# Kernel tuning notes

Hardware: AMD Instinct MI355X
Metric: run time of the kernel (lower is better)

Reference implementation:

```python
import jax, jax.numpy as jnp
import numpy as np

LORA_ALPHA = 32.0
LORA_RANK = 16
SCALE = LORA_ALPHA / LORA_RANK  # 2.0


def setup_inputs() -> dict:
    key = jax.random.key(0)
    ks = jax.random.split(key, 6)
    B, S, I, Q, V, E, R = 4, 4096, 4096, 4096, 1024, 8, LORA_RANK
    return {
        "hidden_states": jax.random.normal(ks[0], (B, S, I), dtype=jnp.float32),
        "router_weight": jax.random.normal(ks[1], (E, I), dtype=jnp.float32) * 0.02,
        "q_lora_a": jax.random.normal(ks[2], (E, I, R), dtype=jnp.float32) * 0.02,
        "q_lora_b": jax.random.normal(ks[3], (E, R, Q), dtype=jnp.float32) * 0.02,
        "v_lora_a": jax.random.normal(ks[4], (E, I, R), dtype=jnp.float32) * 0.02,
        "v_lora_b": jax.random.normal(ks[5], (E, R, V), dtype=jnp.float32) * 0.02,
    }


def reference(hidden_states, router_weight, q_lora_a, q_lora_b, v_lora_a, v_lora_b):
    B, S, I = hidden_states.shape
    E = router_weight.shape[0]
    Q = q_lora_b.shape[-1]
    V = v_lora_b.shape[-1]
    h = hidden_states.reshape(-1, I)  # [T, I]

    # Top-1 routing
    logits = h @ router_weight.T                       # [T, E]
    probs = jax.nn.softmax(logits, axis=-1)
    expert_idx = jnp.argmax(probs, axis=-1)            # [T]
    expert_scores = jnp.max(probs, axis=-1)            # [T]

    # One-hot dispatch folded with per-token score * lora scale
    gate = jax.nn.one_hot(expert_idx, E, dtype=h.dtype) * (expert_scores * SCALE)[:, None]  # [T, E]

    # Low-rank projections for all experts (R is tiny so [T,E,R] is cheap),
    # masked so each token only keeps its selected expert.
    low_q = jnp.einsum('ti,eir->ter', h, q_lora_a) * gate[:, :, None]  # [T, E, R]
    low_v = jnp.einsum('ti,eir->ter', h, v_lora_a) * gate[:, :, None]  # [T, E, R]

    q_delta = jnp.einsum('ter,erq->tq', low_q, q_lora_b)  # [T, Q]
    v_delta = jnp.einsum('ter,erv->tv', low_v, v_lora_b)  # [T, V]

    return q_delta.reshape(B, S, Q), v_delta.reshape(B, S, V)
```

## Files before the change

### kernel.cpp

```cpp
#include <hip/hip_runtime.h>
#include <math.h>

#define TOK_I 4096
#define NE 8
#define NR 16
#define NQ 4096
#define NV 1024
#define LORA_SCALE 2.0f

#define BM2 32
#define KB2 128
#define BM3 32

__global__ __launch_bounds__(256) void qvlora_fused_kernel(
    const float* __restrict__ h, const float* __restrict__ rw,
    const float* __restrict__ qa, const float* __restrict__ qb,
    const float* __restrict__ va, const float* __restrict__ vb,
    float* __restrict__ qout, float* __restrict__ vout)
{
    const int tok  = blockIdx.x;
    const int tid  = threadIdx.x;
    const int lane = tid & 63;
    const int wave = tid >> 6;

    __shared__ float red8[4][8];
    __shared__ float red32[4][32];
    __shared__ float sLow[32];
    __shared__ float sGate;
    __shared__ int   sSel;

    const float4* h4 = (const float4*)(h + (long)tok * TOK_I);
    float4 hreg[4];
#pragma unroll
    for (int k = 0; k < 4; ++k) hreg[k] = h4[tid + 256 * k];

    float lacc[NE];
#pragma unroll
    for (int e = 0; e < NE; ++e) lacc[e] = 0.f;
    const float4* rw4 = (const float4*)rw;
#pragma unroll
    for (int k = 0; k < 4; ++k) {
        float4 hv = hreg[k];
        int f = tid + 256 * k;
#pragma unroll
        for (int e = 0; e < NE; ++e) {
            float4 wv = rw4[e * 1024 + f];
            lacc[e] += hv.x * wv.x + hv.y * wv.y + hv.z * wv.z + hv.w * wv.w;
        }
    }
#pragma unroll
    for (int off = 32; off >= 1; off >>= 1)
#pragma unroll
        for (int e = 0; e < NE; ++e) lacc[e] += __shfl_down(lacc[e], off);
    if (lane == 0)
#pragma unroll
        for (int e = 0; e < NE; ++e) red8[wave][e] = lacc[e];
    __syncthreads();

    if (tid == 0) {
        float lg[NE];
#pragma unroll
        for (int e = 0; e < NE; ++e)
            lg[e] = red8[0][e] + red8[1][e] + red8[2][e] + red8[3][e];
        int best = 0; float mx = lg[0];
#pragma unroll
        for (int e = 1; e < NE; ++e) if (lg[e] > mx) { mx = lg[e]; best = e; }
        float s = 0.f;
#pragma unroll
        for (int e = 0; e < NE; ++e) s += __expf(lg[e] - mx);
        sSel = best; sGate = LORA_SCALE / s;
    }
    __syncthreads();

    const int e = sSel;
    float acc[32];
#pragma unroll
    for (int c = 0; c < 32; ++c) acc[c] = 0.f;
    const float4* qa4 = (const float4*)(qa + (long)e * TOK_I * NR);
    const float4* va4 = (const float4*)(va + (long)e * TOK_I * NR);
#pragma unroll
    for (int k = 0; k < 4; ++k) {
        float4 hv = hreg[k];
        float he[4] = {hv.x, hv.y, hv.z, hv.w};
        int i0 = 4 * (tid + 256 * k);
#pragma unroll
        for (int d = 0; d < 4; ++d) {
            int row4 = (i0 + d) * 4;
#pragma unroll
            for (int r4 = 0; r4 < 4; ++r4) {
                float4 wq = qa4[row4 + r4];
                float4 wv = va4[row4 + r4];
                acc[4*r4+0] += he[d]*wq.x; acc[4*r4+1] += he[d]*wq.y;
                acc[4*r4+2] += he[d]*wq.z; acc[4*r4+3] += he[d]*wq.w;
                acc[16+4*r4+0] += he[d]*wv.x; acc[16+4*r4+1] += he[d]*wv.y;
                acc[16+4*r4+2] += he[d]*wv.z; acc[16+4*r4+3] += he[d]*wv.w;
            }
        }
    }
#pragma unroll
    for (int off = 32; off >= 1; off >>= 1)
#pragma unroll
        for (int c = 0; c < 32; ++c) acc[c] += __shfl_down(acc[c], off);
    if (lane == 0)
#pragma unroll
        for (int c = 0; c < 32; ++c) red32[wave][c] = acc[c];
    __syncthreads();
    if (tid < 32) {
        float v = red32[0][tid] + red32[1][tid] + red32[2][tid] + red32[3][tid];
        sLow[tid] = v * sGate;
    }
    __syncthreads();

    float lq[NR], lv[NR];
#pragma unroll
    for (int r = 0; r < NR; ++r) { lq[r] = sLow[r]; lv[r] = sLow[16 + r]; }
    const float4* qb4 = (const float4*)(qb + (long)e * NR * NQ);
    const float4* vb4 = (const float4*)(vb + (long)e * NR * NV);
    float4* qo4 = (float4*)(qout + (long)tok * NQ);
    float4* vo4 = (float4*)(vout + (long)tok * NV);
    {
        float4 o = {0,0,0,0};
#pragma unroll
        for (int r = 0; r < NR; ++r) {
            float4 w = vb4[r * 256 + tid];
            o.x += lv[r]*w.x; o.y += lv[r]*w.y; o.z += lv[r]*w.z; o.w += lv[r]*w.w;
        }
        vo4[tid] = o;
    }
#pragma unroll
    for (int m = 0; m < 4; ++m) {
        float4 o = {0,0,0,0};
        int f = tid + 256 * m;
#pragma unroll
        for (int r = 0; r < NR; ++r) {
            float4 w = qb4[r * 1024 + f];
            o.x += lq[r]*w.x; o.y += lq[r]*w.y; o.z += lq[r]*w.z; o.w += lq[r]*w.w;
        }
        qo4[f] = o;
    }
}

__global__ __launch_bounds__(256) void router_kernel(
    const float* __restrict__ h, const float* __restrict__ rw,
    float* __restrict__ gate, int* __restrict__ tlist,
    int* __restrict__ count, int T)
{
    const int tok0 = blockIdx.x * 2;
    const int tid  = threadIdx.x;
    const int lane = tid & 63;
    const int wave = tid >> 6;

    __shared__ float red[2][4][NE];

    const float4* h4  = (const float4*)h;
    const float4* rw4 = (const float4*)rw;

    const int tA = tok0;
    const int tB = (tok0 + 1 < T) ? tok0 + 1 : tok0;

    float4 hreg[2][4];
#pragma unroll
    for (int k = 0; k < 4; ++k) {
        hreg[0][k] = h4[(long)tA * 1024 + tid + 256 * k];
        hreg[1][k] = h4[(long)tB * 1024 + tid + 256 * k];
    }

    float lacc[2][NE];
#pragma unroll
    for (int j = 0; j < 2; ++j)
#pragma unroll
        for (int e = 0; e < NE; ++e) lacc[j][e] = 0.f;

#pragma unroll
    for (int k = 0; k < 4; ++k) {
        int f = tid + 256 * k;
        float4 h0 = hreg[0][k], h1 = hreg[1][k];
#pragma unroll
        for (int e = 0; e < NE; ++e) {
            float4 wv = rw4[e * 1024 + f];
            lacc[0][e] += h0.x*wv.x + h0.y*wv.y + h0.z*wv.z + h0.w*wv.w;
            lacc[1][e] += h1.x*wv.x + h1.y*wv.y + h1.z*wv.z + h1.w*wv.w;
        }
    }
#pragma unroll
    for (int off = 32; off >= 1; off >>= 1)
#pragma unroll
        for (int j = 0; j < 2; ++j)
#pragma unroll
            for (int e = 0; e < NE; ++e)
                lacc[j][e] += __shfl_down(lacc[j][e], off);

    if (lane == 0)
#pragma unroll
        for (int j = 0; j < 2; ++j)
#pragma unroll
            for (int e = 0; e < NE; ++e) red[j][wave][e] = lacc[j][e];
    __syncthreads();

    if (tid < 2) {
        int tk = tok0 + tid;
        if (tk < T) {
            float lg[NE];
#pragma unroll
            for (int e = 0; e < NE; ++e)
                lg[e] = red[tid][0][e] + red[tid][1][e] + red[tid][2][e] + red[tid][3][e];
            int best = 0; float mx = lg[0];
#pragma unroll
            for (int e = 1; e < NE; ++e) if (lg[e] > mx) { mx = lg[e]; best = e; }
            float s = 0.f;
#pragma unroll
            for (int e = 0; e < NE; ++e) s += __expf(lg[e] - mx);
            gate[tk] = LORA_SCALE / s;
            int pos = atomicAdd(&count[best], 1);
            tlist[best * T + pos] = tk;
        }
    }
}

__global__ __launch_bounds__(256) void lowrank_kernel(
    const float* __restrict__ h, const float* __restrict__ qa,
    const float* __restrict__ va, const float* __restrict__ gate,
    const int* __restrict__ tlist, const int* __restrict__ count,
    float* __restrict__ low, int T)
{
    const int e   = blockIdx.y;
    const int cnt = count[e];
    const int m0  = blockIdx.x * BM2;
    if (m0 >= cnt) return;
    const int tid = threadIdx.x;

    __shared__ float h_s[KB2][BM2 + 1];
    __shared__ float a_s[KB2][32];
    __shared__ int   tl_s[BM2];
    __shared__ float g_s[BM2];

    if (tid < BM2) {
        int idx = m0 + tid;
        int tk = (idx < cnt) ? tlist[e * T + idx] : -1;
        tl_s[tid] = tk;
        g_s[tid]  = (tk >= 0) ? gate[tk] : 0.f;
    }
    __syncthreads();

    const int m  = tid & 31;
    const int rg = tid >> 5;
    float4 acc = {0.f, 0.f, 0.f, 0.f};

    const float4* h4  = (const float4*)h;
    const float4* qa4 = (const float4*)(qa + (long)e * TOK_I * NR);
    const float4* va4 = (const float4*)(va + (long)e * TOK_I * NR);
    float4* a_s4 = (float4*)a_s;

    const int sm  = tid >> 3;
    const int skq = tid & 7;
    const int stl = tl_s[sm];

    for (int k0 = 0; k0 < TOK_I; k0 += KB2) {
#pragma unroll
        for (int i = 0; i < 4; ++i) {
            int kq = skq + 8 * i;
            float4 hv = (stl >= 0) ? h4[(long)stl * 1024 + (k0 >> 2) + kq]
                                   : make_float4(0.f, 0.f, 0.f, 0.f);
            int kk = kq * 4;
            h_s[kk + 0][sm] = hv.x; h_s[kk + 1][sm] = hv.y;
            h_s[kk + 2][sm] = hv.z; h_s[kk + 3][sm] = hv.w;
        }
#pragma unroll
        for (int i = 0; i < 4; ++i) {
            int lin  = tid * 4 + i;
            int kk   = lin >> 3;
            int slot = lin & 7;
            float4 wv = (slot < 4) ? qa4[(long)(k0 + kk) * 4 + slot]
                                   : va4[(long)(k0 + kk) * 4 + (slot - 4)];
            a_s4[kk * 8 + slot] = wv;
        }
        __syncthreads();
#pragma unroll 8
        for (int k = 0; k < KB2; ++k) {
            float  hv = h_s[k][m];
            float4 av = a_s4[k * 8 + rg];
            acc.x += hv * av.x; acc.y += hv * av.y;
            acc.z += hv * av.z; acc.w += hv * av.w;
        }
        __syncthreads();
    }

    float g = g_s[m];
    acc.x *= g; acc.y *= g; acc.z *= g; acc.w *= g;
    int tk = tl_s[m];
    if (tk >= 0) {
        float4* low4 = (float4*)low;
        low4[(long)tk * 8 + rg] = acc;
    }
}

__global__ __launch_bounds__(256) void expand_kernel(
    const float* __restrict__ low, const float* __restrict__ qb,
    const float* __restrict__ vb, const int* __restrict__ tlist,
    const int* __restrict__ count,
    float* __restrict__ qout, float* __restrict__ vout, int T)
{
    const int e   = blockIdx.y;
    const int cnt = count[e];
    const int m0  = blockIdx.x * BM3;
    if (m0 >= cnt) return;
    const int tid = threadIdx.x;

    __shared__ float lq_s[BM3][NR];
    __shared__ float lv_s[BM3][NR];
    __shared__ int   tl_s[BM3];

    if (tid < BM3) {
        int idx = m0 + tid;
        tl_s[tid] = (idx < cnt) ? tlist[e * T + idx] : -1;
    }
    __syncthreads();
    {
        int mm = tid >> 3, rg = tid & 7;
        int tk = tl_s[mm];
        const float4* low4 = (const float4*)low;
        float4 v = (tk >= 0) ? low4[(long)tk * 8 + rg]
                             : make_float4(0.f, 0.f, 0.f, 0.f);
        if (rg < 4) ((float4*)lq_s[mm])[rg]     = v;
        else        ((float4*)lv_s[mm])[rg - 4] = v;
    }
    __syncthreads();

    const float4* qb4 = (const float4*)(qb + (long)e * NR * NQ);
    const float4* vb4 = (const float4*)(vb + (long)e * NR * NV);
    float4* qo4 = (float4*)qout;
    float4* vo4 = (float4*)vout;

#pragma unroll
    for (int c = 0; c < 4; ++c) {
        int n4 = tid + 256 * c;
        float4 w[NR];
#pragma unroll
        for (int r = 0; r < NR; ++r) w[r] = qb4[r * 1024 + n4];
        for (int mm = 0; mm < BM3; ++mm) {
            int tk = tl_s[mm];
            if (tk < 0) break;
            float4 o = {0.f, 0.f, 0.f, 0.f};
#pragma unroll
            for (int r = 0; r < NR; ++r) {
                float l = lq_s[mm][r];
                o.x += l * w[r].x; o.y += l * w[r].y;
                o.z += l * w[r].z; o.w += l * w[r].w;
            }
            qo4[(long)tk * 1024 + n4] = o;
        }
    }
    {
        int n4 = tid;
        float4 w[NR];
#pragma unroll
        for (int r = 0; r < NR; ++r) w[r] = vb4[r * 256 + n4];
        for (int mm = 0; mm < BM3; ++mm) {
            int tk = tl_s[mm];
            if (tk < 0) break;
            float4 o = {0.f, 0.f, 0.f, 0.f};
#pragma unroll
            for (int r = 0; r < NR; ++r) {
                float l = lv_s[mm][r];
                o.x += l * w[r].x; o.y += l * w[r].y;
                o.z += l * w[r].z; o.w += l * w[r].w;
            }
            vo4[(long)tk * 256 + n4] = o;
        }
    }
}

extern "C" void kernel_launch(void* const* d_in, const int* in_sizes, int n_in,
                              void* d_out, int out_size, void* d_ws, size_t ws_size,
                              hipStream_t stream) {
    const float* h  = (const float*)d_in[0];
    const float* rw = (const float*)d_in[1];
    const float* qa = (const float*)d_in[2];
    const float* qb = (const float*)d_in[3];
    const float* va = (const float*)d_in[4];
    const float* vb = (const float*)d_in[5];
    float* out = (float*)d_out;

    const int T = in_sizes[0] / TOK_I;
    float* qout = out;
    float* vout = out + (long)T * NQ;

    size_t off_count = 0;
    size_t off_gate  = 256;
    size_t off_tlist = off_gate + (size_t)T * 4;
    size_t off_low   = off_tlist + (size_t)NE * T * 4;
    size_t req       = off_low + (size_t)T * 32 * 4;

    if (ws_size < req || d_ws == nullptr) {
        qvlora_fused_kernel<<<T, 256, 0, stream>>>(h, rw, qa, qb, va, vb, qout, vout);
        return;
    }

    char*  ws    = (char*)d_ws;
    int*   count = (int*)(ws + off_count);
    float* gate  = (float*)(ws + off_gate);
    int*   tlist = (int*)(ws + off_tlist);
    float* low   = (float*)(ws + off_low);

    hipMemsetAsync(count, 0, 256, stream);
    router_kernel<<<(T + 1) / 2, 256, 0, stream>>>(h, rw, gate, tlist, count, T);
    dim3 g2((T + BM2 - 1) / BM2, NE);
    lowrank_kernel<<<g2, 256, 0, stream>>>(h, qa, va, gate, tlist, count, low, T);
    dim3 g3((T + BM3 - 1) / BM3, NE);
    expand_kernel<<<g3, 256, 0, stream>>>(low, qb, vb, tlist, count, qout, vout, T);
}
```

Before: 826.5 us.

## Split-K lowrank with register-tiled accumulators and split expand over output columns

The lowrank kernel now processes 128 tokens per block with 128 threads, each computing a 4-token by 8-rank register tile, and splits the reduction dimension four ways across grid z. Partial sums go to a workspace buffer. The expand kernel sums the four partials, applies the gate, and is itself split across z so each block handles one quarter of the Q columns or the V columns. The aim is more reuse of the adapter weights per load and more parallel blocks. The cost is extra partial-sum traffic, a larger workspace, and the weight loads in expand being repeated per z slice.

```diff
diff --git a/kernel.cpp b/kernel.cpp
--- a/kernel.cpp
+++ b/kernel.cpp
@@ -8,9 +8,17 @@
 #define NV 1024
 #define LORA_SCALE 2.0f
 
-#define BM2 32
-#define KB2 128
+#define BM2 128
+#define KB2 64
+#define KS  4
 #define BM3 32
+
+__device__ __forceinline__ void f4axpy(float4& o, float s, const float4& w) {
+    o.x += s * w.x;
+    o.y += s * w.y;
+    o.z += s * w.z;
+    o.w += s * w.w;
+}
 
 __global__ __launch_bounds__(256) void qvlora_fused_kernel(
     const float* __restrict__ h, const float* __restrict__ rw,
@@ -119,22 +127,22 @@
     float4* qo4 = (float4*)(qout + (long)tok * NQ);
     float4* vo4 = (float4*)(vout + (long)tok * NV);
     {
-        float4 o = {0,0,0,0};
+        float4 o = {0.f, 0.f, 0.f, 0.f};
 #pragma unroll
         for (int r = 0; r < NR; ++r) {
             float4 w = vb4[r * 256 + tid];
-            o.x += lv[r]*w.x; o.y += lv[r]*w.y; o.z += lv[r]*w.z; o.w += lv[r]*w.w;
+            f4axpy(o, lv[r], w);
         }
         vo4[tid] = o;
     }
 #pragma unroll
     for (int m = 0; m < 4; ++m) {
-        float4 o = {0,0,0,0};
+        float4 o = {0.f, 0.f, 0.f, 0.f};
         int f = tid + 256 * m;
 #pragma unroll
         for (int r = 0; r < NR; ++r) {
             float4 w = qb4[r * 1024 + f];
-            o.x += lq[r]*w.x; o.y += lq[r]*w.y; o.z += lq[r]*w.z; o.w += lq[r]*w.w;
+            f4axpy(o, lq[r], w);
         }
         qo4[f] = o;
     }
@@ -217,97 +225,127 @@
     }
 }
 
-__global__ __launch_bounds__(256) void lowrank_kernel(
+__global__ __launch_bounds__(128) void lowrank_kernel(
     const float* __restrict__ h, const float* __restrict__ qa,
-    const float* __restrict__ va, const float* __restrict__ gate,
+    const float* __restrict__ va,
     const int* __restrict__ tlist, const int* __restrict__ count,
-    float* __restrict__ low, int T)
+    float* __restrict__ lowp, int T)
 {
     const int e   = blockIdx.y;
     const int cnt = count[e];
     const int m0  = blockIdx.x * BM2;
     if (m0 >= cnt) return;
+    const int z   = blockIdx.z;
     const int tid = threadIdx.x;
 
-    __shared__ float h_s[KB2][BM2 + 1];
+    __shared__ float h_s[KB2][BM2 + 4];
     __shared__ float a_s[KB2][32];
     __shared__ int   tl_s[BM2];
-    __shared__ float g_s[BM2];
-
-    if (tid < BM2) {
+
+    {
         int idx = m0 + tid;
-        int tk = (idx < cnt) ? tlist[e * T + idx] : -1;
-        tl_s[tid] = tk;
-        g_s[tid]  = (tk >= 0) ? gate[tk] : 0.f;
-    }
-    __syncthreads();
-
-    const int m  = tid & 31;
-    const int rg = tid >> 5;
-    float4 acc = {0.f, 0.f, 0.f, 0.f};
+        tl_s[tid] = (idx < cnt) ? tlist[e * T + idx] : -1;
+    }
+    __syncthreads();
+
+    const int tg = tid & 31;
+    const int og = tid >> 5;
+    const int kq = tid & 15;
+    const int tq = tid >> 4;
+
+    float4 accA0 = {0,0,0,0}, accA1 = {0,0,0,0}, accA2 = {0,0,0,0}, accA3 = {0,0,0,0};
+    float4 accB0 = {0,0,0,0}, accB1 = {0,0,0,0}, accB2 = {0,0,0,0}, accB3 = {0,0,0,0};
 
     const float4* h4  = (const float4*)h;
     const float4* qa4 = (const float4*)(qa + (long)e * TOK_I * NR);
     const float4* va4 = (const float4*)(va + (long)e * TOK_I * NR);
+    float4* h_s4 = (float4*)h_s;
     float4* a_s4 = (float4*)a_s;
 
-    const int sm  = tid >> 3;
-    const int skq = tid & 7;
-    const int stl = tl_s[sm];
-
-    for (int k0 = 0; k0 < TOK_I; k0 += KB2) {
+    const int kbase = z * (TOK_I / KS);
+
+    for (int k0 = kbase; k0 < kbase + TOK_I / KS; k0 += KB2) {
+#pragma unroll
+        for (int p = 0; p < 4; ++p) {
+            int tquad = tq + 8 * p;
+            float4 hv0, hv1, hv2, hv3;
+            {
+                int t0 = tl_s[4 * tquad + 0];
+                int t1 = tl_s[4 * tquad + 1];
+                int t2 = tl_s[4 * tquad + 2];
+                int t3 = tl_s[4 * tquad + 3];
+                long cb = (long)(k0 >> 2) + kq;
+                hv0 = (t0 >= 0) ? h4[(long)t0 * 1024 + cb] : make_float4(0.f,0.f,0.f,0.f);
+                hv1 = (t1 >= 0) ? h4[(long)t1 * 1024 + cb] : make_float4(0.f,0.f,0.f,0.f);
+                hv2 = (t2 >= 0) ? h4[(long)t2 * 1024 + cb] : make_float4(0.f,0.f,0.f,0.f);
+                hv3 = (t3 >= 0) ? h4[(long)t3 * 1024 + cb] : make_float4(0.f,0.f,0.f,0.f);
+            }
+            h_s4[(4*kq + 0) * 33 + tquad] = make_float4(hv0.x, hv1.x, hv2.x, hv3.x);
+            h_s4[(4*kq + 1) * 33 + tquad] = make_float4(hv0.y, hv1.y, hv2.y, hv3.y);
+            h_s4[(4*kq + 2) * 33 + tquad] = make_float4(hv0.z, hv1.z, hv2.z, hv3.z);
+            h_s4[(4*kq + 3) * 33 + tquad] = make_float4(hv0.w, hv1.w, hv2.w, hv3.w);
+        }
 #pragma unroll
         for (int i = 0; i < 4; ++i) {
-            int kq = skq + 8 * i;
-            float4 hv = (stl >= 0) ? h4[(long)stl * 1024 + (k0 >> 2) + kq]
-                                   : make_float4(0.f, 0.f, 0.f, 0.f);
-            int kk = kq * 4;
-            h_s[kk + 0][sm] = hv.x; h_s[kk + 1][sm] = hv.y;
-            h_s[kk + 2][sm] = hv.z; h_s[kk + 3][sm] = hv.w;
-        }
-#pragma unroll
-        for (int i = 0; i < 4; ++i) {
-            int lin  = tid * 4 + i;
-            int kk   = lin >> 3;
-            int slot = lin & 7;
-            float4 wv = (slot < 4) ? qa4[(long)(k0 + kk) * 4 + slot]
-                                   : va4[(long)(k0 + kk) * 4 + (slot - 4)];
-            a_s4[kk * 8 + slot] = wv;
+            int lin = tid + 128 * i;
+            int kk  = lin >> 3;
+            int s   = lin & 7;
+            float4 wv = (s < 4) ? qa4[(long)(k0 + kk) * 4 + s]
+                                : va4[(long)(k0 + kk) * 4 + (s - 4)];
+            a_s4[kk * 8 + s] = wv;
         }
         __syncthreads();
-#pragma unroll 8
+
+#pragma unroll 4
         for (int k = 0; k < KB2; ++k) {
-            float  hv = h_s[k][m];
-            float4 av = a_s4[k * 8 + rg];
-            acc.x += hv * av.x; acc.y += hv * av.y;
-            acc.z += hv * av.z; acc.w += hv * av.w;
+            float4 hv = h_s4[k * 33 + tg];
+            float4 a0 = a_s4[k * 8 + og * 2];
+            float4 a1 = a_s4[k * 8 + og * 2 + 1];
+            f4axpy(accA0, hv.x, a0); f4axpy(accB0, hv.x, a1);
+            f4axpy(accA1, hv.y, a0); f4axpy(accB1, hv.y, a1);
+            f4axpy(accA2, hv.z, a0); f4axpy(accB2, hv.z, a1);
+            f4axpy(accA3, hv.w, a0); f4axpy(accB3, hv.w, a1);
         }
         __syncthreads();
     }
 
-    float g = g_s[m];
-    acc.x *= g; acc.y *= g; acc.z *= g; acc.w *= g;
-    int tk = tl_s[m];
-    if (tk >= 0) {
-        float4* low4 = (float4*)low;
-        low4[(long)tk * 8 + rg] = acc;
+    float4* lp4 = (float4*)lowp;
+    {
+        int tk = tl_s[4 * tg + 0];
+        if (tk >= 0) { long b = ((long)z * T + tk) * 8 + og * 2;
+                       lp4[b] = accA0; lp4[b + 1] = accB0; }
+    }
+    {
+        int tk = tl_s[4 * tg + 1];
+        if (tk >= 0) { long b = ((long)z * T + tk) * 8 + og * 2;
+                       lp4[b] = accA1; lp4[b + 1] = accB1; }
+    }
+    {
+        int tk = tl_s[4 * tg + 2];
+        if (tk >= 0) { long b = ((long)z * T + tk) * 8 + og * 2;
+                       lp4[b] = accA2; lp4[b + 1] = accB2; }
+    }
+    {
+        int tk = tl_s[4 * tg + 3];
+        if (tk >= 0) { long b = ((long)z * T + tk) * 8 + og * 2;
+                       lp4[b] = accA3; lp4[b + 1] = accB3; }
     }
 }
 
 __global__ __launch_bounds__(256) void expand_kernel(
-    const float* __restrict__ low, const float* __restrict__ qb,
-    const float* __restrict__ vb, const int* __restrict__ tlist,
-    const int* __restrict__ count,
+    const float* __restrict__ lowp, const float* __restrict__ qb,
+    const float* __restrict__ vb, const float* __restrict__ gate,
+    const int* __restrict__ tlist, const int* __restrict__ count,
     float* __restrict__ qout, float* __restrict__ vout, int T)
 {
     const int e   = blockIdx.y;
     const int cnt = count[e];
     const int m0  = blockIdx.x * BM3;
     if (m0 >= cnt) return;
+    const int z   = blockIdx.z;
     const int tid = threadIdx.x;
 
-    __shared__ float lq_s[BM3][NR];
-    __shared__ float lv_s[BM3][NR];
+    __shared__ float ls[BM3][32];
     __shared__ int   tl_s[BM3];
 
     if (tid < BM3) {
@@ -316,55 +354,54 @@
     }
     __syncthreads();
     {
-        int mm = tid >> 3, rg = tid & 7;
+        int mm = tid >> 3, s = tid & 7;
         int tk = tl_s[mm];
-        const float4* low4 = (const float4*)low;
-        float4 v = (tk >= 0) ? low4[(long)tk * 8 + rg]
-                             : make_float4(0.f, 0.f, 0.f, 0.f);
-        if (rg < 4) ((float4*)lq_s[mm])[rg]     = v;
-        else        ((float4*)lv_s[mm])[rg - 4] = v;
-    }
-    __syncthreads();
-
-    const float4* qb4 = (const float4*)(qb + (long)e * NR * NQ);
-    const float4* vb4 = (const float4*)(vb + (long)e * NR * NV);
-    float4* qo4 = (float4*)qout;
-    float4* vo4 = (float4*)vout;
-
-#pragma unroll
-    for (int c = 0; c < 4; ++c) {
-        int n4 = tid + 256 * c;
+        float4 v = {0.f, 0.f, 0.f, 0.f};
+        if (tk >= 0) {
+            const float4* lp4 = (const float4*)lowp;
+            long b0 = ((long)0 * T + tk) * 8 + s;
+            long b1 = ((long)1 * T + tk) * 8 + s;
+            long b2 = ((long)2 * T + tk) * 8 + s;
+            long b3 = ((long)3 * T + tk) * 8 + s;
+            float4 p0 = lp4[b0], p1 = lp4[b1], p2 = lp4[b2], p3 = lp4[b3];
+            float g = gate[tk];
+            v.x = ((p0.x + p1.x) + (p2.x + p3.x)) * g;
+            v.y = ((p0.y + p1.y) + (p2.y + p3.y)) * g;
+            v.z = ((p0.z + p1.z) + (p2.z + p3.z)) * g;
+            v.w = ((p0.w + p1.w) + (p2.w + p3.w)) * g;
+        }
+        ((float4*)ls[mm])[s] = v;
+    }
+    __syncthreads();
+
+    if (z < 4) {
+        int n4 = z * 256 + tid;
+        const float4* qb4 = (const float4*)(qb + (long)e * NR * NQ);
         float4 w[NR];
 #pragma unroll
         for (int r = 0; r < NR; ++r) w[r] = qb4[r * 1024 + n4];
+        float4* qo4 = (float4*)qout;
         for (int mm = 0; mm < BM3; ++mm) {
             int tk = tl_s[mm];
             if (tk < 0) break;
             float4 o = {0.f, 0.f, 0.f, 0.f};
 #pragma unroll
-            for (int r = 0; r < NR; ++r) {
-                float l = lq_s[mm][r];
-                o.x += l * w[r].x; o.y += l * w[r].y;
-                o.z += l * w[r].z; o.w += l * w[r].w;
-            }
+            for (int r = 0; r < NR; ++r) { float l = ls[mm][r]; f4axpy(o, l, w[r]); }
             qo4[(long)tk * 1024 + n4] = o;
         }
-    }
-    {
+    } else {
         int n4 = tid;
+        const float4* vb4 = (const float4*)(vb + (long)e * NR * NV);
         float4 w[NR];
 #pragma unroll
         for (int r = 0; r < NR; ++r) w[r] = vb4[r * 256 + n4];
+        float4* vo4 = (float4*)vout;
         for (int mm = 0; mm < BM3; ++mm) {
             int tk = tl_s[mm];
             if (tk < 0) break;
             float4 o = {0.f, 0.f, 0.f, 0.f};
 #pragma unroll
-            for (int r = 0; r < NR; ++r) {
-                float l = lv_s[mm][r];
-                o.x += l * w[r].x; o.y += l * w[r].y;
-                o.z += l * w[r].z; o.w += l * w[r].w;
-            }
+            for (int r = 0; r < NR; ++r) { float l = ls[mm][16 + r]; f4axpy(o, l, w[r]); }
             vo4[(long)tk * 256 + n4] = o;
         }
     }
@@ -388,8 +425,8 @@
     size_t off_count = 0;
     size_t off_gate  = 256;
     size_t off_tlist = off_gate + (size_t)T * 4;
-    size_t off_low   = off_tlist + (size_t)NE * T * 4;
-    size_t req       = off_low + (size_t)T * 32 * 4;
+    size_t off_lowp  = off_tlist + (size_t)NE * T * 4;
+    size_t req       = off_lowp + (size_t)KS * T * 32 * 4;
 
     if (ws_size < req || d_ws == nullptr) {
         qvlora_fused_kernel<<<T, 256, 0, stream>>>(h, rw, qa, qb, va, vb, qout, vout);
@@ -400,12 +437,12 @@
     int*   count = (int*)(ws + off_count);
     float* gate  = (float*)(ws + off_gate);
     int*   tlist = (int*)(ws + off_tlist);
-    float* low   = (float*)(ws + off_low);
+    float* lowp  = (float*)(ws + off_lowp);
 
     hipMemsetAsync(count, 0, 256, stream);
     router_kernel<<<(T + 1) / 2, 256, 0, stream>>>(h, rw, gate, tlist, count, T);
-    dim3 g2((T + BM2 - 1) / BM2, NE);
-    lowrank_kernel<<<g2, 256, 0, stream>>>(h, qa, va, gate, tlist, count, low, T);
-    dim3 g3((T + BM3 - 1) / BM3, NE);
-    expand_kernel<<<g3, 256, 0, stream>>>(low, qb, vb, tlist, count, qout, vout, T);
-}
+    dim3 g2((T + BM2 - 1) / BM2, NE, KS);
+    lowrank_kernel<<<g2, 128, 0, stream>>>(h, qa, va, tlist, count, lowp, T);
+    dim3 g3((T + BM3 - 1) / BM3, NE, 5);
+    expand_kernel<<<g3, 256, 0, stream>>>(lowp, qb, vb, gate, tlist, count, qout, vout, T);
+}
```

New measurement: 906.6 us. 1.1x slower.
